# Kernel optimization log

Measured on AMD Instinct MI355X. Metric: run time of the kernel, lower is better.

Reference implementation:

```python
import jax, jax.numpy as jnp
import numpy as np

NL, D, DI, N, R, K = 4, 256, 512, 16, 16, 4  # layers, d_model, d_inner, d_state, dt_rank, conv kernel


def setup_inputs() -> dict:
    key = jax.random.key(0)
    ks = jax.random.split(key, 10)
    b, nc, nt = 8, 256, 64
    xc = jax.random.normal(ks[0], (b, nc, D), jnp.float32)
    xt = jax.random.normal(ks[1], (b, nt, D), jnp.float32)
    ln_g = jnp.ones((NL, D), jnp.float32)
    ln_b = jnp.zeros((NL, D), jnp.float32)
    W_in = jax.random.normal(ks[2], (NL, D, 2 * DI), jnp.float32) * (D ** -0.5)
    W_conv = jax.random.normal(ks[3], (NL, DI, 1, K), jnp.float32) * 0.2
    b_conv = jnp.zeros((NL, DI), jnp.float32)
    W_x = jax.random.normal(ks[4], (NL, DI, R + 2 * N), jnp.float32) * (DI ** -0.5)
    W_dt = jax.random.normal(ks[5], (NL, R, DI), jnp.float32) * (R ** -0.5)
    b_dt = jax.random.normal(ks[6], (NL, DI), jnp.float32) * 0.5 - 4.0  # softplus ~ 0.02
    A_log = jnp.broadcast_to(jnp.log(jnp.arange(1, N + 1, dtype=jnp.float32)), (NL, DI, N)).copy()
    Dp = jnp.ones((NL, DI), jnp.float32)
    W_out = jax.random.normal(ks[7], (NL, DI, D), jnp.float32) * (DI ** -0.5)
    return dict(xc=xc, xt=xt, ln_g=ln_g, ln_b=ln_b, W_in=W_in, W_conv=W_conv, b_conv=b_conv,
                W_x=W_x, W_dt=W_dt, b_dt=b_dt, A_log=A_log, Dp=Dp, W_out=W_out)


def _mamba_layer(x, g, beta, Wi, Wc, bc, Wx, Wdt, bdt, Alog, Dvec, Wo):
    # x: [B, L, D]; pre-LN residual Mamba-1 block
    mu = jnp.mean(x, axis=-1, keepdims=True)
    var = jnp.var(x, axis=-1, keepdims=True)
    h = (x - mu) * jax.lax.rsqrt(var + 1e-5) * g + beta
    xz = h @ Wi                              # [B, L, 2*DI]
    xp, z = xz[..., :DI], xz[..., DI:]
    # causal depthwise conv1d
    xcv = jax.lax.conv_general_dilated(xp.transpose(0, 2, 1), Wc, (1,), [(K - 1, 0)],
                                       feature_group_count=DI,
                                       dimension_numbers=('NCH', 'OIH', 'NCH'))
    xcv = jax.nn.silu(xcv.transpose(0, 2, 1) + bc)  # [B, L, DI]
    dbl = xcv @ Wx                           # [B, L, R+2N]
    dt = jax.nn.softplus(dbl[..., :R] @ Wdt + bdt)   # [B, L, DI]
    Bm = dbl[..., R:R + N]                   # [B, L, N]
    Cm = dbl[..., R + N:]                    # [B, L, N]
    A = -jnp.exp(Alog)                       # [DI, N]

    def step(hst, inp):
        x_t, dt_t, b_t, c_t = inp            # [B,DI],[B,DI],[B,N],[B,N]
        dA = jnp.exp(dt_t[:, :, None] * A)   # [B, DI, N]
        hst = dA * hst + (dt_t * x_t)[:, :, None] * b_t[:, None, :]
        return hst, jnp.einsum('bdn,bn->bd', hst, c_t)

    h0 = jnp.zeros((x.shape[0], DI, N), x.dtype)
    _, ys = jax.lax.scan(step, h0, (xcv.transpose(1, 0, 2), dt.transpose(1, 0, 2),
                                    Bm.transpose(1, 0, 2), Cm.transpose(1, 0, 2)))
    y = ys.transpose(1, 0, 2) + xcv * Dvec
    y = y * jax.nn.silu(z)
    return x + y @ Wo


def reference(xc, xt, ln_g, ln_b, W_in, W_conv, b_conv, W_x, W_dt, b_dt, A_log, Dp, W_out):
    b, nc, d = xc.shape
    nt = xt.shape[1]
    # replicate context per target token: [b*nt, nc+1, d]
    xr = jnp.broadcast_to(xc[:, None], (b, nt, nc, d)).reshape(b * nt, nc, d)
    x = jnp.concatenate([xr, xt.reshape(b * nt, 1, d)], axis=1)
    for i in range(NL):
        x = _mamba_layer(x, ln_g[i], ln_b[i], W_in[i], W_conv[i], b_conv[i],
                         W_x[i], W_dt[i], b_dt[i], A_log[i], Dp[i], W_out[i])
    return x[:, -1, :].reshape(b, nt, d)
```

## Files before the change

### kernel.cpp

```cpp
#include <hip/hip_runtime.h>
#include <hip/hip_bf16.h>

#define D_     256
#define TWO_DI 1024
#define DI_    512
#define NSTATE 16
#define RR     16
#define NDBL   48
#define BSEQ   8
#define NC     256
#define NCHUNK 16
#define CLEN   16
#define CTX    2048
#define TGT    512

typedef __attribute__((ext_vector_type(8))) short short8v;
typedef __attribute__((ext_vector_type(8))) unsigned short ushort8v;
typedef __attribute__((ext_vector_type(4))) float floatx4;

__device__ __forceinline__ float siluf(float x) { return x / (1.f + __expf(-x)); }
__device__ __forceinline__ float softplusf(float x) {
  return fmaxf(x, 0.f) + log1pf(__expf(-fabsf(x)));
}
__device__ __forceinline__ unsigned short f2bf(float x) {
  unsigned u = __float_as_uint(x);
  u += 0x7fffu + ((u >> 16) & 1u);
  return (unsigned short)(u >> 16);
}
__device__ __forceinline__ float bf2f(unsigned short b) {
  return __uint_as_float((unsigned)b << 16);
}

__global__ __launch_bounds__(256) void prep_all(
    const float* __restrict__ W_in, const float* __restrict__ W_o,
    const float* __restrict__ W_x, const float* __restrict__ Alog,
    const float* __restrict__ W_dt,
    unsigned short* __restrict__ Wint, unsigned short* __restrict__ Wot,
    unsigned short* __restrict__ Wxt, float* __restrict__ Aneg,
    float* __restrict__ WdtT)
{
  __shared__ float tile[32][33];
  int b = blockIdx.x;
  const float* src; unsigned short* dst; int R, C, cx, ry;
  if (b < 1024) {
    int z = b >> 8, t = b & 255; cx = t & 31; ry = t >> 5; R = 256; C = 1024;
    src = W_in + (size_t)z * R * C; dst = Wint + (size_t)z * R * C;
  } else if (b < 1536) {
    int bb = b - 1024; int z = bb >> 7, t = bb & 127; cx = t & 7; ry = t >> 3; R = 512; C = 256;
    src = W_o + (size_t)z * R * C; dst = Wot + (size_t)z * R * C;
  } else if (b < 1664) {
    int bb = b - 1536; int z = bb >> 5, t = bb & 31; cx = t & 1; ry = t >> 1; R = 512; C = 48;
    src = W_x + (size_t)z * R * C; dst = Wxt + (size_t)z * R * C;
  } else if (b < 1792) {
    int i = (b - 1664) * 256 + threadIdx.x;
    if (i < 4 * DI_ * NSTATE) Aneg[i] = -__expf(Alog[i]);
    return;
  } else {
    int i = (b - 1792) * 256 + threadIdx.x;
    int z = i >> 13, rem = i & 8191, c = rem >> 4, r = rem & 15;
    WdtT[i] = W_dt[(size_t)z * RR * DI_ + r * DI_ + c];
    return;
  }
  int c0 = cx * 32, r0 = ry * 32;
  int tx = threadIdx.x & 31, ty = threadIdx.x >> 5;
#pragma unroll
  for (int i = 0; i < 4; ++i) {
    int r = r0 + ty + i * 8;
    tile[ty + i * 8][tx] = (r < R && c0 + tx < C) ? src[(size_t)r * C + c0 + tx] : 0.f;
  }
  __syncthreads();
#pragma unroll
  for (int i = 0; i < 4; ++i) {
    int c = c0 + ty + i * 8;
    if (c < C && r0 + tx < R)
      dst[(size_t)c * R + r0 + tx] = f2bf(tile[tx][ty + i * 8]);
  }
}

__device__ __forceinline__ void ln_body(int bx, const float* __restrict__ x,
    const float* __restrict__ g, const float* __restrict__ be,
    unsigned short* __restrict__ out, int rows)
{
  int wid = threadIdx.x >> 6, lane = threadIdx.x & 63;
  int row = bx * 4 + wid;
  if (row >= rows) return;
  const float4 v = *reinterpret_cast<const float4*>(&x[(size_t)row * D_ + lane * 4]);
  float s  = v.x + v.y + v.z + v.w;
  float sq = v.x * v.x + v.y * v.y + v.z * v.z + v.w * v.w;
#pragma unroll
  for (int off = 32; off; off >>= 1) {
    s  += __shfl_xor(s, off);
    sq += __shfl_xor(sq, off);
  }
  float mu   = s * (1.f / D_);
  float var  = sq * (1.f / D_) - mu * mu;
  float rstd = rsqrtf(var + 1e-5f);
  const float4 gv = *reinterpret_cast<const float4*>(&g[lane * 4]);
  const float4 bv = *reinterpret_cast<const float4*>(&be[lane * 4]);
  ushort4 o;
  o.x = f2bf((v.x - mu) * rstd * gv.x + bv.x);
  o.y = f2bf((v.y - mu) * rstd * gv.y + bv.y);
  o.z = f2bf((v.z - mu) * rstd * gv.z + bv.z);
  o.w = f2bf((v.w - mu) * rstd * gv.w + bv.w);
  *reinterpret_cast<ushort4*>(&out[(size_t)row * D_ + lane * 4]) = o;
}

__global__ __launch_bounds__(256) void ln_kern(const float* __restrict__ x,
    const float* __restrict__ g, const float* __restrict__ be,
    unsigned short* __restrict__ out, int rows)
{
  ln_body(blockIdx.x, x, g, be, out, rows);
}

__global__ __launch_bounds__(256) void fused_ln(
    const float* __restrict__ xA, const float* __restrict__ gA,
    const float* __restrict__ bA, unsigned short* __restrict__ oA,
    const float* __restrict__ xB, const float* __restrict__ gB,
    const float* __restrict__ bB, unsigned short* __restrict__ oB)
{
  if (blockIdx.x < CTX / 4) ln_body(blockIdx.x, xA, gA, bA, oA, CTX);
  else                      ln_body(blockIdx.x - CTX / 4, xB, gB, bB, oB, TGT);
}

template<int EPI>
__device__ __forceinline__ void gemm_body(
    unsigned short (*As)[72], unsigned short (*Bs)[72], int bx, int by,
    const unsigned short* __restrict__ A, const unsigned short* __restrict__ Bt,
    const float* __restrict__ resid, float* __restrict__ C, int M, int N, int K,
    const float* __restrict__ cconv, const float* __restrict__ Wc4,
    unsigned short* __restrict__ xcv_bf, float* __restrict__ zbuf)
{
  int tid = threadIdx.x;
  int n0 = bx * 64, m0 = by * 64;
  int w = tid >> 6, lane = tid & 63;
  int lr = lane & 15, kq = lane >> 4;
  int wr = w >> 1, wc = w & 1;
  int srow = tid >> 2, schunk = (tid & 3) * 16;
  const unsigned short* Ap = &A[(size_t)(m0 + srow) * K + schunk];
  const unsigned short* Bp = &Bt[(size_t)(n0 + srow) * K + schunk];
  ushort8v a0 = *reinterpret_cast<const ushort8v*>(Ap);
  ushort8v a1 = *reinterpret_cast<const ushort8v*>(Ap + 8);
  ushort8v b0 = *reinterpret_cast<const ushort8v*>(Bp);
  ushort8v b1 = *reinterpret_cast<const ushort8v*>(Bp + 8);
  floatx4 acc[2][2] = {};
  for (int k0 = 0; k0 < K; k0 += 64) {
    __syncthreads();
    *reinterpret_cast<ushort8v*>(&As[srow][schunk])     = a0;
    *reinterpret_cast<ushort8v*>(&As[srow][schunk + 8]) = a1;
    *reinterpret_cast<ushort8v*>(&Bs[srow][schunk])     = b0;
    *reinterpret_cast<ushort8v*>(&Bs[srow][schunk + 8]) = b1;
    __syncthreads();
    if (k0 + 64 < K) {
      a0 = *reinterpret_cast<const ushort8v*>(Ap + k0 + 64);
      a1 = *reinterpret_cast<const ushort8v*>(Ap + k0 + 72);
      b0 = *reinterpret_cast<const ushort8v*>(Bp + k0 + 64);
      b1 = *reinterpret_cast<const ushort8v*>(Bp + k0 + 72);
    }
#pragma unroll
    for (int ks = 0; ks < 2; ++ks) {
      short8v af[2], bf2v[2];
#pragma unroll
      for (int f = 0; f < 2; ++f)
        af[f] = *reinterpret_cast<const short8v*>(&As[wr * 32 + f * 16 + lr][ks * 32 + kq * 8]);
#pragma unroll
      for (int g2 = 0; g2 < 2; ++g2)
        bf2v[g2] = *reinterpret_cast<const short8v*>(&Bs[wc * 32 + g2 * 16 + lr][ks * 32 + kq * 8]);
#pragma unroll
      for (int f = 0; f < 2; ++f)
#pragma unroll
        for (int g2 = 0; g2 < 2; ++g2)
          acc[f][g2] = __builtin_amdgcn_mfma_f32_16x16x32_bf16(af[f], bf2v[g2], acc[f][g2], 0, 0, 0);
    }
  }
#pragma unroll
  for (int f = 0; f < 2; ++f)
#pragma unroll
    for (int g2 = 0; g2 < 2; ++g2) {
      int col = n0 + wc * 32 + g2 * 16 + lr;
#pragma unroll
      for (int r = 0; r < 4; ++r) {
        int row = m0 + wr * 32 + f * 16 + kq * 4 + r;
        float v = acc[f][g2][r];
        if (EPI == 0) {
          if (resid) v += resid[(size_t)row * N + col];
          C[(size_t)row * N + col] = v;
        } else {
          int b = row >> 6;
          if (col < DI_) {
            float sv = siluf(cconv[b * DI_ + col] + v * Wc4[col * 4 + 3]);
            xcv_bf[(size_t)row * DI_ + col] = f2bf(sv);
          } else {
            zbuf[(size_t)row * DI_ + (col - DI_)] = v;
          }
        }
      }
    }
}

template<int EPI>
__global__ __launch_bounds__(256) void gemm_bf16(
    const unsigned short* __restrict__ A, const unsigned short* __restrict__ Bt,
    const float* __restrict__ resid, float* __restrict__ C, int M, int N, int K,
    const float* __restrict__ cconv, const float* __restrict__ Wc4,
    unsigned short* __restrict__ xcv_bf, float* __restrict__ zbuf)
{
  __shared__ unsigned short As[64][72];
  __shared__ unsigned short Bs[64][72];
  gemm_body<EPI>(As, Bs, blockIdx.x, blockIdx.y, A, Bt, resid, C, M, N, K,
                 cconv, Wc4, xcv_bf, zbuf);
}

__global__ __launch_bounds__(256) void fused_gemm_in(
    const unsigned short* __restrict__ Aa, const unsigned short* __restrict__ Bta,
    float* __restrict__ Ca,
    const unsigned short* __restrict__ Ab, const unsigned short* __restrict__ Btb,
    const float* __restrict__ cconv, const float* __restrict__ Wc4,
    unsigned short* __restrict__ xcv_bf, float* __restrict__ zbuf)
{
  __shared__ unsigned short As[64][72];
  __shared__ unsigned short Bs[64][72];
  int f = blockIdx.x;
  if (f < 512)
    gemm_body<0>(As, Bs, f & 15, f >> 4, Aa, Bta, nullptr, Ca, CTX, TWO_DI, D_,
                 nullptr, nullptr, nullptr, nullptr);
  else {
    f -= 512;
    gemm_body<1>(As, Bs, f & 15, f >> 4, Ab, Btb, nullptr, nullptr, TGT, TWO_DI, D_,
                 cconv, Wc4, xcv_bf, zbuf);
  }
}

__device__ __forceinline__ void gemm_s_body(int bx, int by,
    const unsigned short* __restrict__ A, const unsigned short* __restrict__ Bt,
    const float* __restrict__ resid, float* __restrict__ C, int M, int N, int K)
{
  __shared__ unsigned short As[32][72];
  __shared__ unsigned short Bs[32][72];
  int tid = threadIdx.x;
  int n0 = bx * 32, m0 = by * 32;
  int w = tid >> 6, lane = tid & 63;
  int lr = lane & 15, kq = lane >> 4;
  int wr = w >> 1, wc = w & 1;
  int srow = tid >> 3, schunk = (tid & 7) * 8;
  const unsigned short* Ap = &A[(size_t)(m0 + srow) * K + schunk];
  const unsigned short* Bp = &Bt[(size_t)(n0 + srow) * K + schunk];
  ushort8v a0 = *reinterpret_cast<const ushort8v*>(Ap);
  ushort8v b0 = *reinterpret_cast<const ushort8v*>(Bp);
  floatx4 acc = {};
  for (int k0 = 0; k0 < K; k0 += 64) {
    __syncthreads();
    *reinterpret_cast<ushort8v*>(&As[srow][schunk]) = a0;
    *reinterpret_cast<ushort8v*>(&Bs[srow][schunk]) = b0;
    __syncthreads();
    if (k0 + 64 < K) {
      a0 = *reinterpret_cast<const ushort8v*>(Ap + k0 + 64);
      b0 = *reinterpret_cast<const ushort8v*>(Bp + k0 + 64);
    }
#pragma unroll
    for (int ks = 0; ks < 2; ++ks) {
      short8v af = *reinterpret_cast<const short8v*>(&As[wr * 16 + lr][ks * 32 + kq * 8]);
      short8v bf = *reinterpret_cast<const short8v*>(&Bs[wc * 16 + lr][ks * 32 + kq * 8]);
      acc = __builtin_amdgcn_mfma_f32_16x16x32_bf16(af, bf, acc, 0, 0, 0);
    }
  }
  int col = n0 + wc * 16 + lr;
#pragma unroll
  for (int r = 0; r < 4; ++r) {
    int row = m0 + wr * 16 + kq * 4 + r;
    float v = acc[r];
    if (resid) v += resid[(size_t)row * N + col];
    C[(size_t)row * N + col] = v;
  }
}

__global__ __launch_bounds__(256) void gemm_s(
    const unsigned short* __restrict__ A, const unsigned short* __restrict__ Bt,
    const float* __restrict__ resid, float* __restrict__ C, int M, int N, int K)
{
  gemm_s_body(blockIdx.x, blockIdx.y, A, Bt, resid, C, M, N, K);
}

__device__ __forceinline__ void conv_body_lean(int blk,
    const float* __restrict__ xz, const float* __restrict__ Wc,
    const float* __restrict__ bc, const unsigned short* __restrict__ Wxt,
    const float* __restrict__ WdtT, const float* __restrict__ bdt,
    unsigned short* __restrict__ xcvb, float* __restrict__ dtb,
    float* __restrict__ dblg, float* __restrict__ cconv)
{
  __shared__ unsigned short xcs[16][528];
  __shared__ float dbl_s[16][48];
  int seq = blk >> 4, ch = blk & 15;
  int tok0 = blk * 16;
  int tid = threadIdx.x;
  int base = ch * 16;
#pragma unroll
  for (int hh = 0; hh < 2; ++hh) {
    int c = tid + hh * 256;
    const float4 wv = *reinterpret_cast<const float4*>(&Wc[c * 4]);
    float bcv = bc[c];
    const float* xzs = &xz[(size_t)(seq * NC) * TWO_DI + c];
    float r[19];
#pragma unroll
    for (int i = 0; i < 19; ++i) {
      int tl = base - 3 + i;
      r[i] = (tl >= 0) ? xzs[(size_t)tl * TWO_DI] : 0.f;
    }
#pragma unroll
    for (int t = 0; t < 16; ++t) {
      float acc = bcv + r[t] * wv.x + r[t + 1] * wv.y + r[t + 2] * wv.z + r[t + 3] * wv.w;
      unsigned short sv = f2bf(siluf(acc));
      xcs[t][c] = sv;
      xcvb[(size_t)(tok0 + t) * DI_ + c] = sv;
    }
    if (ch == 15)
      cconv[seq * DI_ + c] = bcv + r[16] * wv.x + r[17] * wv.y + r[18] * wv.z;
  }
  __syncthreads();
  int w = tid >> 6, lane = tid & 63, lr = lane & 15, kq = lane >> 4;
  if (w < 3) {
    floatx4 acc = {};
#pragma unroll
    for (int kc = 0; kc < 16; ++kc) {
      short8v bb = *reinterpret_cast<const short8v*>(&Wxt[(size_t)(w * 16 + lr) * DI_ + kc * 32 + kq * 8]);
      short8v aa = *reinterpret_cast<const short8v*>(&xcs[lr][kc * 32 + kq * 8]);
      acc = __builtin_amdgcn_mfma_f32_16x16x32_bf16(aa, bb, acc, 0, 0, 0);
    }
#pragma unroll
    for (int r2 = 0; r2 < 4; ++r2) {
      int t = kq * 4 + r2, col = w * 16 + lr;
      dbl_s[t][col] = acc[r2];
      dblg[(size_t)(tok0 + t) * NDBL + col] = acc[r2];
    }
  }
  __syncthreads();
#pragma unroll
  for (int hh = 0; hh < 2; ++hh) {
    int c = tid + hh * 256;
    float wr_[16];
    const float4* wt4 = reinterpret_cast<const float4*>(&WdtT[c * 16]);
#pragma unroll
    for (int q = 0; q < 4; ++q) {
      float4 v4 = wt4[q];
      wr_[q * 4] = v4.x; wr_[q * 4 + 1] = v4.y; wr_[q * 4 + 2] = v4.z; wr_[q * 4 + 3] = v4.w;
    }
    float bv = bdt[c];
#pragma unroll
    for (int t = 0; t < 16; ++t) {
      float accd = bv;
#pragma unroll
      for (int r2 = 0; r2 < 16; ++r2) accd += dbl_s[t][r2] * wr_[r2];
      dtb[(size_t)(tok0 + t) * DI_ + c] = softplusf(accd);
    }
  }
}

__global__ __launch_bounds__(256) void conv_lean_kern(
    const float* __restrict__ xz, const float* __restrict__ Wc,
    const float* __restrict__ bc, const unsigned short* __restrict__ Wxt,
    const float* __restrict__ WdtT, const float* __restrict__ bdt,
    unsigned short* __restrict__ xcvb, float* __restrict__ dtb,
    float* __restrict__ dblg, float* __restrict__ cconv)
{
  conv_body_lean(blockIdx.x, xz, Wc, bc, Wxt, WdtT, bdt, xcvb, dtb, dblg, cconv);
}

__device__ __forceinline__ void sp_body(int b,
    const float* __restrict__ dblg, const unsigned short* __restrict__ xcvb,
    const float* __restrict__ dtb, const float* __restrict__ Aneg,
    float* __restrict__ Sb, float* __restrict__ Pb)
{
  int dg = b & 31, sc = b >> 5;
  int tid = threadIdx.x;
  int tt = tid >> 4, cc = tid & 15;
  int tok0 = sc * CLEN;
  __shared__ float dts[16][17], xs[16][17], Bs[16][17];
  dts[tt][cc] = dtb[(size_t)(tok0 + tt) * DI_ + dg * 16 + cc];
  xs[tt][cc]  = bf2f(xcvb[(size_t)(tok0 + tt) * DI_ + dg * 16 + cc]);
  Bs[tt][cc]  = dblg[(size_t)(tok0 + tt) * NDBL + RR + cc];
  __syncthreads();
  int dl = tt, n = cc;
  int d = dg * 16 + dl;
  float A = Aneg[d * NSTATE + n];
  float Bn[16];
#pragma unroll
  for (int t = 0; t < CLEN; ++t) Bn[t] = Bs[t][n];
  float h = 0.f, p = 1.f;
#pragma unroll
  for (int t = 0; t < CLEN; ++t) {
    float dtv = dts[t][dl];
    float dA  = __expf(dtv * A);
    h = fmaf(dA, h, dtv * xs[t][dl] * Bn[t]);
    p *= dA;
  }
  size_t o = ((size_t)sc * DI_ + d) * NSTATE + n;
  Sb[o] = h; Pb[o] = p;
}

__global__ __launch_bounds__(256) void sp_kern(
    const float* __restrict__ dblg, const unsigned short* __restrict__ xcvb,
    const float* __restrict__ dtb, const float* __restrict__ Aneg,
    float* __restrict__ Sb, float* __restrict__ Pb)
{
  sp_body(blockIdx.x, dblg, xcvb, dtb, Aneg, Sb, Pb);
}

__global__ __launch_bounds__(256) void fused_sp_gout(
    const unsigned short* __restrict__ Ag, const unsigned short* __restrict__ Btg,
    const float* __restrict__ residg, float* __restrict__ Cg,
    const float* __restrict__ dblg, const unsigned short* __restrict__ xcvb,
    const float* __restrict__ dtb, const float* __restrict__ Aneg,
    float* __restrict__ Sb, float* __restrict__ Pb)
{
  if (blockIdx.x < 128) {
    int f = blockIdx.x;
    gemm_s_body(f & 7, f >> 3, Ag, Btg, residg, Cg, TGT, D_, DI_);
  } else {
    sp_body(blockIdx.x - 128, dblg, xcvb, dtb, Aneg, Sb, Pb);
  }
}

__global__ __launch_bounds__(256) void scan_fin(
    const float* __restrict__ dblg, const unsigned short* __restrict__ xcvb,
    const float* __restrict__ xz, const float* __restrict__ dtb,
    const float* __restrict__ Sb, const float* __restrict__ Pb,
    const float* __restrict__ Aneg, const float* __restrict__ Dp,
    unsigned short* __restrict__ yb, float* __restrict__ hstate)
{
  int b = blockIdx.x;
  int dg = b & 31, sc = b >> 5;
  int seq = sc >> 4, chunk = sc & 15;
  int tid = threadIdx.x;
  int tt = tid >> 4, cc = tid & 15;
  int tok0 = sc * CLEN;
  __shared__ float dts[16][17], xs[16][17], zs[16][17], Bs[16][17], Cs[16][17], ys[16][17];
  dts[tt][cc] = dtb[(size_t)(tok0 + tt) * DI_ + dg * 16 + cc];
  xs[tt][cc]  = bf2f(xcvb[(size_t)(tok0 + tt) * DI_ + dg * 16 + cc]);
  zs[tt][cc]  = xz[(size_t)(tok0 + tt) * TWO_DI + DI_ + dg * 16 + cc];
  Bs[tt][cc]  = dblg[(size_t)(tok0 + tt) * NDBL + RR + cc];
  Cs[tt][cc]  = dblg[(size_t)(tok0 + tt) * NDBL + RR + NSTATE + cc];
  __syncthreads();
  int dl = tt, n = cc;
  int d = dg * 16 + dl;
  float A  = Aneg[d * NSTATE + n];
  float Dv = Dp[d];
  float Bn[16], Cn[16];
#pragma unroll
  for (int t = 0; t < CLEN; ++t) { Bn[t] = Bs[t][n]; Cn[t] = Cs[t][n]; }
  float h = 0.f;
  for (int c2 = 0; c2 < chunk; ++c2) {
    size_t o = ((size_t)(seq * NCHUNK + c2) * DI_ + d) * NSTATE + n;
    h = fmaf(Pb[o], h, Sb[o]);
  }
#pragma unroll
  for (int t = 0; t < CLEN; ++t) {
    float dtv = dts[t][dl];
    float xv  = xs[t][dl];
    float dA  = __expf(dtv * A);
    h = fmaf(dA, h, dtv * xv * Bn[t]);
    float p = h * Cn[t];
    p += __shfl_xor(p, 1); p += __shfl_xor(p, 2);
    p += __shfl_xor(p, 4); p += __shfl_xor(p, 8);
    if (n == 0) ys[t][dl] = (p + xv * Dv) * siluf(zs[t][dl]);
  }
  __syncthreads();
  yb[(size_t)(tok0 + tt) * DI_ + dg * 16 + cc] = f2bf(ys[tt][cc]);
  if (chunk == NCHUNK - 1)
    hstate[(size_t)seq * DI_ * NSTATE + d * NSTATE + n] = h;
}

__device__ __forceinline__ void ssm_body(int blk,
    const unsigned short* __restrict__ xcv_bf, const float* __restrict__ zbuf,
    const unsigned short* __restrict__ Wx, const float* __restrict__ WdtT_l,
    const float* __restrict__ bdt_l, const float* __restrict__ An_l,
    const float* __restrict__ Dp_l, const float* __restrict__ hs,
    unsigned short* __restrict__ ybf)
{
  __shared__ float dbl_s[16][48];
  int tg = blk >> 3, cg = blk & 7;
  int tok0 = tg * 16;
  int b = tg >> 2;
  int tid = threadIdx.x;
  int w = tid >> 6, lane = tid & 63, lr = lane & 15, kq = lane >> 4;
  if (w < 3) {
    floatx4 acc = {};
#pragma unroll
    for (int kc = 0; kc < 16; ++kc) {
      short8v bb = *reinterpret_cast<const short8v*>(&Wx[(size_t)(w * 16 + lr) * DI_ + kc * 32 + kq * 8]);
      short8v aa = *reinterpret_cast<const short8v*>(&xcv_bf[(size_t)(tok0 + lr) * DI_ + kc * 32 + kq * 8]);
      acc = __builtin_amdgcn_mfma_f32_16x16x32_bf16(aa, bb, acc, 0, 0, 0);
    }
#pragma unroll
    for (int r = 0; r < 4; ++r)
      dbl_s[kq * 4 + r][w * 16 + lr] = acc[r];
  }
  __syncthreads();
  int c = cg * 64 + (tid & 63);
  int t0 = (tid >> 6) * 4;
  float wdt_r[16], An[16], hr[16];
  const float4* wt4 = reinterpret_cast<const float4*>(&WdtT_l[c * 16]);
  const float4* An4 = reinterpret_cast<const float4*>(&An_l[c * NSTATE]);
  const float4* hr4 = reinterpret_cast<const float4*>(&hs[(size_t)b * DI_ * NSTATE + c * NSTATE]);
#pragma unroll
  for (int q = 0; q < 4; ++q) {
    float4 wv = wt4[q]; wdt_r[q*4]=wv.x; wdt_r[q*4+1]=wv.y; wdt_r[q*4+2]=wv.z; wdt_r[q*4+3]=wv.w;
    float4 a = An4[q]; An[q*4]=a.x; An[q*4+1]=a.y; An[q*4+2]=a.z; An[q*4+3]=a.w;
    float4 hv = hr4[q]; hr[q*4]=hv.x; hr[q*4+1]=hv.y; hr[q*4+2]=hv.z; hr[q*4+3]=hv.w;
  }
  float Dv = Dp_l[c], bv = bdt_l[c];
#pragma unroll
  for (int tt = 0; tt < 4; ++tt) {
    int t = t0 + tt;
    float accd = bv;
#pragma unroll
    for (int r = 0; r < 16; ++r) accd += dbl_s[t][r] * wdt_r[r];
    float dtv = softplusf(accd);
    float xv = bf2f(xcv_bf[(size_t)(tok0 + t) * DI_ + c]);
    float coef = dtv * xv;
    float y = 0.f;
#pragma unroll
    for (int n = 0; n < 16; ++n) {
      float hn = fmaf(__expf(dtv * An[n]), hr[n], coef * dbl_s[t][RR + n]);
      y = fmaf(hn, dbl_s[t][RR + NSTATE + n], y);
    }
    float yv = (y + xv * Dv) * siluf(zbuf[(size_t)(tok0 + t) * DI_ + c]);
    ybf[(size_t)(tok0 + t) * DI_ + c] = f2bf(yv);
  }
}

__global__ __launch_bounds__(256) void tgt_ssm2(
    const unsigned short* __restrict__ xcv_bf, const float* __restrict__ zbuf,
    const unsigned short* __restrict__ Wx, const float* __restrict__ WdtT_l,
    const float* __restrict__ bdt_l, const float* __restrict__ An_l,
    const float* __restrict__ Dp_l, const float* __restrict__ hs,
    unsigned short* __restrict__ ybf)
{
  ssm_body(blockIdx.x, xcv_bf, zbuf, Wx, WdtT_l, bdt_l, An_l, Dp_l, hs, ybf);
}

__global__ __launch_bounds__(256) void fused_conv_ssm(
    const float* __restrict__ xz, const float* __restrict__ Wc,
    const float* __restrict__ bc, const unsigned short* __restrict__ WxtA,
    const float* __restrict__ WdtTA, const float* __restrict__ bdtA,
    unsigned short* __restrict__ xcvb, float* __restrict__ dtb,
    float* __restrict__ dblg, float* __restrict__ cconv,
    const unsigned short* __restrict__ xcv_bfB, const float* __restrict__ zbufB,
    const unsigned short* __restrict__ WxB, const float* __restrict__ WdtTB,
    const float* __restrict__ bdtB, const float* __restrict__ AnB,
    const float* __restrict__ DpB, const float* __restrict__ hsB,
    unsigned short* __restrict__ ybfB)
{
  if (blockIdx.x < BSEQ * NCHUNK)
    conv_body_lean(blockIdx.x, xz, Wc, bc, WxtA, WdtTA, bdtA,
                   xcvb, dtb, dblg, cconv);
  else
    ssm_body(blockIdx.x - BSEQ * NCHUNK, xcv_bfB, zbufB, WxB, WdtTB, bdtB,
             AnB, DpB, hsB, ybfB);
}

extern "C" void kernel_launch(void* const* d_in, const int* in_sizes, int n_in,
                              void* d_out, int out_size, void* d_ws, size_t ws_size,
                              hipStream_t stream)
{
  const float* xc   = (const float*)d_in[0];
  const float* xt   = (const float*)d_in[1];
  const float* ln_g = (const float*)d_in[2];
  const float* ln_b = (const float*)d_in[3];
  const float* W_in = (const float*)d_in[4];
  const float* W_cv = (const float*)d_in[5];
  const float* b_cv = (const float*)d_in[6];
  const float* W_x  = (const float*)d_in[7];
  const float* W_dt = (const float*)d_in[8];
  const float* b_dt = (const float*)d_in[9];
  const float* Alog = (const float*)d_in[10];
  const float* Dp   = (const float*)d_in[11];
  const float* W_o  = (const float*)d_in[12];
  float* out = (float*)d_out;

  float* ws = (float*)d_ws;
  size_t off = 0;
  auto alloc = [&](size_t n) { float* p = ws + off; off += n; return p; };
  float* xz     = alloc((size_t)CTX * TWO_DI);
  float* dtb    = alloc((size_t)CTX * DI_);
  float* dblg   = alloc((size_t)CTX * NDBL);
  float* xcur   = alloc((size_t)CTX * D_);
  float* Sb     = alloc((size_t)BSEQ * NCHUNK * DI_ * NSTATE);
  float* Pb     = alloc((size_t)BSEQ * NCHUNK * DI_ * NSTATE);
  float* cconvT = alloc((size_t)4 * BSEQ * DI_);
  float* hst    = alloc((size_t)4 * BSEQ * DI_ * NSTATE);
  float* Aneg   = alloc((size_t)4 * DI_ * NSTATE);
  float* WdtT   = alloc((size_t)4 * DI_ * RR);
  float* zbufB  = alloc((size_t)TGT * DI_);
  float* xtb    = alloc((size_t)TGT * D_);
  unsigned short* hbuf_bf = (unsigned short*)alloc((size_t)CTX * D_ / 2);
  unsigned short* hbufB   = (unsigned short*)alloc((size_t)TGT * D_ / 2);
  unsigned short* xcvb    = (unsigned short*)alloc((size_t)CTX * DI_ / 2);
  unsigned short* yb_bf   = (unsigned short*)alloc((size_t)CTX * DI_ / 2);
  unsigned short* xcv_bfB = (unsigned short*)alloc((size_t)TGT * DI_ / 2);
  unsigned short* y_bfB   = (unsigned short*)alloc((size_t)TGT * DI_ / 2);
  unsigned short* Wint    = (unsigned short*)alloc((size_t)4 * TWO_DI * D_ / 2);
  unsigned short* Wot     = (unsigned short*)alloc((size_t)4 * D_ * DI_ / 2);
  unsigned short* Wxt     = (unsigned short*)alloc((size_t)4 * NDBL * DI_ / 2);
  if (off * sizeof(float) > ws_size) return;

  prep_all<<<1920, 256, 0, stream>>>(W_in, W_o, W_x, Alog, W_dt,
                                     Wint, Wot, Wxt, Aneg, WdtT);

  ln_kern<<<CTX / 4, 256, 0, stream>>>(xc, ln_g, ln_b, hbuf_bf, CTX);
  gemm_bf16<0><<<dim3(TWO_DI / 64, CTX / 64), 256, 0, stream>>>(
      hbuf_bf, Wint, nullptr, xz, CTX, TWO_DI, D_, nullptr, nullptr, nullptr, nullptr);
  conv_lean_kern<<<BSEQ * NCHUNK, 256, 0, stream>>>(
      xz, W_cv, b_cv, Wxt, WdtT, b_dt, xcvb, dtb, dblg, cconvT);
  sp_kern<<<BSEQ * NCHUNK * 32, 256, 0, stream>>>(dblg, xcvb, dtb, Aneg, Sb, Pb);
  scan_fin<<<BSEQ * NCHUNK * 32, 256, 0, stream>>>(
      dblg, xcvb, xz, dtb, Sb, Pb, Aneg, Dp, yb_bf, hst);
  gemm_bf16<0><<<dim3(D_ / 64, CTX / 64), 256, 0, stream>>>(
      yb_bf, Wot, xc, xcur, CTX, D_, DI_, nullptr, nullptr, nullptr, nullptr);

  for (int l = 0; l < 3; ++l) {
    int la = l + 1;
    const float* xinB = (l == 0) ? xt : xtb;
    fused_ln<<<CTX / 4 + TGT / 4, 256, 0, stream>>>(
        xcur, ln_g + la * D_, ln_b + la * D_, hbuf_bf,
        xinB, ln_g + l * D_,  ln_b + l * D_,  hbufB);
    fused_gemm_in<<<512 + 128, 256, 0, stream>>>(
        hbuf_bf, Wint + (size_t)la * TWO_DI * D_, xz,
        hbufB,   Wint + (size_t)l * TWO_DI * D_,
        cconvT + (size_t)l * BSEQ * DI_, W_cv + l * DI_ * 4, xcv_bfB, zbufB);
    fused_conv_ssm<<<BSEQ * NCHUNK + 256, 256, 0, stream>>>(
        xz, W_cv + la * DI_ * 4, b_cv + la * DI_, Wxt + (size_t)la * NDBL * DI_,
        WdtT + (size_t)la * DI_ * RR, b_dt + la * DI_,
        xcvb, dtb, dblg, cconvT + (size_t)la * BSEQ * DI_,
        xcv_bfB, zbufB, Wxt + (size_t)l * NDBL * DI_, WdtT + (size_t)l * DI_ * RR,
        b_dt + l * DI_, Aneg + l * DI_ * NSTATE, Dp + l * DI_,
        hst + (size_t)l * BSEQ * DI_ * NSTATE, y_bfB);
    fused_sp_gout<<<128 + BSEQ * NCHUNK * 32, 256, 0, stream>>>(
        y_bfB, Wot + (size_t)l * D_ * DI_, xinB, xtb,
        dblg, xcvb, dtb, Aneg + la * DI_ * NSTATE, Sb, Pb);
    scan_fin<<<BSEQ * NCHUNK * 32, 256, 0, stream>>>(
        dblg, xcvb, xz, dtb, Sb, Pb, Aneg + la * DI_ * NSTATE, Dp + la * DI_,
        yb_bf, hst + (size_t)la * BSEQ * DI_ * NSTATE);
    if (la < 3)
      gemm_bf16<0><<<dim3(D_ / 64, CTX / 64), 256, 0, stream>>>(
          yb_bf, Wot + (size_t)la * D_ * DI_, xcur, xcur, CTX, D_, DI_,
          nullptr, nullptr, nullptr, nullptr);
  }

  ln_kern<<<TGT / 4, 256, 0, stream>>>(xtb, ln_g + 3 * D_, ln_b + 3 * D_, hbufB, TGT);
  gemm_bf16<1><<<dim3(TWO_DI / 64, TGT / 64), 256, 0, stream>>>(
      hbufB, Wint + (size_t)3 * TWO_DI * D_, nullptr, nullptr, TGT, TWO_DI, D_,
      cconvT + (size_t)3 * BSEQ * DI_, W_cv + 3 * DI_ * 4, xcv_bfB, zbufB);
  tgt_ssm2<<<256, 256, 0, stream>>>(xcv_bfB, zbufB,
      Wxt + (size_t)3 * NDBL * DI_, WdtT + (size_t)3 * DI_ * RR, b_dt + 3 * DI_,
      Aneg + 3 * DI_ * NSTATE, Dp + 3 * DI_,
      hst + (size_t)3 * BSEQ * DI_ * NSTATE, y_bfB);
  gemm_s<<<dim3(D_ / 32, TGT / 32), 256, 0, stream>>>(
      y_bfB, Wot + (size_t)3 * D_ * DI_, xtb, out, TGT, D_, DI_);
}
```

Before: 306.3 us.

## Fuse layernorm into input GEMM and replace chunked scan with sequential full scan

LayerNorm is folded into the input-projection GEMM: each block recomputes row mean and variance from fp32 activations and normalizes on the fly while staging A tiles, which removes the separate LN launches and the bf16 hidden buffers. The two-pass chunked scan (per-chunk partial states, then a prefix combine) is replaced by one kernel per sequence and channel group that walks all 16 chunks in order, prefetching the next chunk's inputs into registers. This removes a kernel launch and the Sb/Pb state traffic per layer. In exchange it cuts scan parallelism from 4096 to 256 blocks and makes every N-tile block of the GEMM recompute the LN statistics.

```diff
diff --git a/kernel.cpp b/kernel.cpp
--- a/kernel.cpp
+++ b/kernel.cpp
@@ -77,61 +77,161 @@
   }
 }
 
-__device__ __forceinline__ void ln_body(int bx, const float* __restrict__ x,
-    const float* __restrict__ g, const float* __restrict__ be,
-    unsigned short* __restrict__ out, int rows)
-{
-  int wid = threadIdx.x >> 6, lane = threadIdx.x & 63;
-  int row = bx * 4 + wid;
-  if (row >= rows) return;
-  const float4 v = *reinterpret_cast<const float4*>(&x[(size_t)row * D_ + lane * 4]);
-  float s  = v.x + v.y + v.z + v.w;
-  float sq = v.x * v.x + v.y * v.y + v.z * v.z + v.w * v.w;
-#pragma unroll
-  for (int off = 32; off; off >>= 1) {
-    s  += __shfl_xor(s, off);
-    sq += __shfl_xor(sq, off);
-  }
-  float mu   = s * (1.f / D_);
-  float var  = sq * (1.f / D_) - mu * mu;
-  float rstd = rsqrtf(var + 1e-5f);
-  const float4 gv = *reinterpret_cast<const float4*>(&g[lane * 4]);
-  const float4 bv = *reinterpret_cast<const float4*>(&be[lane * 4]);
-  ushort4 o;
-  o.x = f2bf((v.x - mu) * rstd * gv.x + bv.x);
-  o.y = f2bf((v.y - mu) * rstd * gv.y + bv.y);
-  o.z = f2bf((v.z - mu) * rstd * gv.z + bv.z);
-  o.w = f2bf((v.w - mu) * rstd * gv.w + bv.w);
-  *reinterpret_cast<ushort4*>(&out[(size_t)row * D_ + lane * 4]) = o;
-}
-
-__global__ __launch_bounds__(256) void ln_kern(const float* __restrict__ x,
-    const float* __restrict__ g, const float* __restrict__ be,
-    unsigned short* __restrict__ out, int rows)
-{
-  ln_body(blockIdx.x, x, g, be, out, rows);
-}
-
-__global__ __launch_bounds__(256) void fused_ln(
-    const float* __restrict__ xA, const float* __restrict__ gA,
-    const float* __restrict__ bA, unsigned short* __restrict__ oA,
-    const float* __restrict__ xB, const float* __restrict__ gB,
-    const float* __restrict__ bB, unsigned short* __restrict__ oB)
-{
-  if (blockIdx.x < CTX / 4) ln_body(blockIdx.x, xA, gA, bA, oA, CTX);
-  else                      ln_body(blockIdx.x - CTX / 4, xB, gB, bB, oB, TGT);
-}
-
 template<int EPI>
-__device__ __forceinline__ void gemm_body(
-    unsigned short (*As)[72], unsigned short (*Bs)[72], int bx, int by,
-    const unsigned short* __restrict__ A, const unsigned short* __restrict__ Bt,
-    const float* __restrict__ resid, float* __restrict__ C, int M, int N, int K,
+__device__ __forceinline__ void gemm_in_ln_body(
+    unsigned short (*As)[72], unsigned short (*Bs)[72],
+    float* gs, float* bs, int bx, int by,
+    const float* __restrict__ X, const float* __restrict__ g,
+    const float* __restrict__ be, const unsigned short* __restrict__ Bt,
+    float* __restrict__ C, int N,
     const float* __restrict__ cconv, const float* __restrict__ Wc4,
     unsigned short* __restrict__ xcv_bf, float* __restrict__ zbuf)
 {
+  const int K = D_;
   int tid = threadIdx.x;
   int n0 = bx * 64, m0 = by * 64;
+  int w = tid >> 6, lane = tid & 63;
+  int lr = lane & 15, kq = lane >> 4;
+  int wr = w >> 1, wc = w & 1;
+  int srow = tid >> 2, schunk = (tid & 3) * 16;
+  const float* Apf = &X[(size_t)(m0 + srow) * K];
+  {
+    const float4* xr = reinterpret_cast<const float4*>(&Apf[(tid & 3) * 64]);
+    float s = 0.f, sq = 0.f;
+#pragma unroll
+    for (int i = 0; i < 16; ++i) {
+      float4 v = xr[i];
+      s += v.x + v.y + v.z + v.w;
+      sq += v.x * v.x + v.y * v.y + v.z * v.z + v.w * v.w;
+    }
+    s += __shfl_xor(s, 1);  s += __shfl_xor(s, 2);
+    sq += __shfl_xor(sq, 1); sq += __shfl_xor(sq, 2);
+    float mu = s * (1.f / K);
+    float rstd = rsqrtf(sq * (1.f / K) - mu * mu + 1e-5f);
+    gs[tid] = g[tid]; bs[tid] = be[tid];
+    const unsigned short* Bp = &Bt[(size_t)(n0 + srow) * K + schunk];
+    float4 af[4];
+#pragma unroll
+    for (int i = 0; i < 4; ++i)
+      af[i] = *reinterpret_cast<const float4*>(&Apf[schunk + i * 4]);
+    ushort8v b0 = *reinterpret_cast<const ushort8v*>(Bp);
+    ushort8v b1 = *reinterpret_cast<const ushort8v*>(Bp + 8);
+    floatx4 acc[2][2] = {};
+    for (int k0 = 0; k0 < K; k0 += 64) {
+      __syncthreads();
+      {
+        int cb = k0 + schunk;
+        ushort8v o0, o1;
+#pragma unroll
+        for (int i = 0; i < 4; ++i) {
+          float4 v = af[i];
+          unsigned short e0 = f2bf((v.x - mu) * rstd * gs[cb + i * 4 + 0] + bs[cb + i * 4 + 0]);
+          unsigned short e1 = f2bf((v.y - mu) * rstd * gs[cb + i * 4 + 1] + bs[cb + i * 4 + 1]);
+          unsigned short e2 = f2bf((v.z - mu) * rstd * gs[cb + i * 4 + 2] + bs[cb + i * 4 + 2]);
+          unsigned short e3 = f2bf((v.w - mu) * rstd * gs[cb + i * 4 + 3] + bs[cb + i * 4 + 3]);
+          if (i < 2) { o0[i*4] = (short)e0; o0[i*4+1] = (short)e1; o0[i*4+2] = (short)e2; o0[i*4+3] = (short)e3; }
+          else { int j = (i-2)*4; o1[j] = (short)e0; o1[j+1] = (short)e1; o1[j+2] = (short)e2; o1[j+3] = (short)e3; }
+        }
+        *reinterpret_cast<ushort8v*>(&As[srow][schunk])     = o0;
+        *reinterpret_cast<ushort8v*>(&As[srow][schunk + 8]) = o1;
+      }
+      *reinterpret_cast<ushort8v*>(&Bs[srow][schunk])     = b0;
+      *reinterpret_cast<ushort8v*>(&Bs[srow][schunk + 8]) = b1;
+      __syncthreads();
+      if (k0 + 64 < K) {
+#pragma unroll
+        for (int i = 0; i < 4; ++i)
+          af[i] = *reinterpret_cast<const float4*>(&Apf[k0 + 64 + schunk + i * 4]);
+        b0 = *reinterpret_cast<const ushort8v*>(Bp + k0 + 64);
+        b1 = *reinterpret_cast<const ushort8v*>(Bp + k0 + 72);
+      }
+#pragma unroll
+      for (int ks = 0; ks < 2; ++ks) {
+        short8v af2[2], bf2v[2];
+#pragma unroll
+        for (int f = 0; f < 2; ++f)
+          af2[f] = *reinterpret_cast<const short8v*>(&As[wr * 32 + f * 16 + lr][ks * 32 + kq * 8]);
+#pragma unroll
+        for (int g2 = 0; g2 < 2; ++g2)
+          bf2v[g2] = *reinterpret_cast<const short8v*>(&Bs[wc * 32 + g2 * 16 + lr][ks * 32 + kq * 8]);
+#pragma unroll
+        for (int f = 0; f < 2; ++f)
+#pragma unroll
+          for (int g2 = 0; g2 < 2; ++g2)
+            acc[f][g2] = __builtin_amdgcn_mfma_f32_16x16x32_bf16(af2[f], bf2v[g2], acc[f][g2], 0, 0, 0);
+      }
+    }
+#pragma unroll
+    for (int f = 0; f < 2; ++f)
+#pragma unroll
+      for (int g2 = 0; g2 < 2; ++g2) {
+        int col = n0 + wc * 32 + g2 * 16 + lr;
+#pragma unroll
+        for (int r = 0; r < 4; ++r) {
+          int row = m0 + wr * 32 + f * 16 + kq * 4 + r;
+          float v = acc[f][g2][r];
+          if (EPI == 0) {
+            C[(size_t)row * N + col] = v;
+          } else {
+            int bb = row >> 6;
+            if (col < DI_) {
+              float sv = siluf(cconv[bb * DI_ + col] + v * Wc4[col * 4 + 3]);
+              xcv_bf[(size_t)row * DI_ + col] = f2bf(sv);
+            } else {
+              zbuf[(size_t)row * DI_ + (col - DI_)] = v;
+            }
+          }
+        }
+      }
+  }
+}
+
+template<int EPI>
+__global__ __launch_bounds__(256) void gemm_in_ln(
+    const float* __restrict__ X, const float* __restrict__ g,
+    const float* __restrict__ be, const unsigned short* __restrict__ Bt,
+    float* __restrict__ C,
+    const float* __restrict__ cconv, const float* __restrict__ Wc4,
+    unsigned short* __restrict__ xcv_bf, float* __restrict__ zbuf)
+{
+  __shared__ unsigned short As[64][72];
+  __shared__ unsigned short Bs[64][72];
+  __shared__ float gs[256], bs[256];
+  gemm_in_ln_body<EPI>(As, Bs, gs, bs, blockIdx.x, blockIdx.y, X, g, be, Bt,
+                       C, TWO_DI, cconv, Wc4, xcv_bf, zbuf);
+}
+
+__global__ __launch_bounds__(256) void fused_gemm_in_ln(
+    const float* __restrict__ Xa, const float* __restrict__ ga,
+    const float* __restrict__ ba, float* __restrict__ Ca,
+    const unsigned short* __restrict__ Bta,
+    const float* __restrict__ Xb, const float* __restrict__ gb,
+    const float* __restrict__ bb, const unsigned short* __restrict__ Btb,
+    const float* __restrict__ cconv, const float* __restrict__ Wc4,
+    unsigned short* __restrict__ xcv_bf, float* __restrict__ zbuf)
+{
+  __shared__ unsigned short As[64][72];
+  __shared__ unsigned short Bs[64][72];
+  __shared__ float gs[256], bs[256];
+  int f = blockIdx.x;
+  if (f < 512)
+    gemm_in_ln_body<0>(As, Bs, gs, bs, f & 15, f >> 4, Xa, ga, ba, Bta,
+                       Ca, TWO_DI, nullptr, nullptr, nullptr, nullptr);
+  else {
+    f -= 512;
+    gemm_in_ln_body<1>(As, Bs, gs, bs, f & 15, f >> 4, Xb, gb, bb, Btb,
+                       nullptr, TWO_DI, cconv, Wc4, xcv_bf, zbuf);
+  }
+}
+
+__global__ __launch_bounds__(256) void gemm_out(
+    const unsigned short* __restrict__ A, const unsigned short* __restrict__ Bt,
+    const float* __restrict__ resid, float* __restrict__ C, int N, int K)
+{
+  __shared__ unsigned short As[64][72];
+  __shared__ unsigned short Bs[64][72];
+  int tid = threadIdx.x;
+  int n0 = blockIdx.x * 64, m0 = blockIdx.y * 64;
   int w = tid >> 6, lane = tid & 63;
   int lr = lane & 15, kq = lane >> 4;
   int wr = w >> 1, wc = w & 1;
@@ -180,59 +280,15 @@
 #pragma unroll
       for (int r = 0; r < 4; ++r) {
         int row = m0 + wr * 32 + f * 16 + kq * 4 + r;
-        float v = acc[f][g2][r];
-        if (EPI == 0) {
-          if (resid) v += resid[(size_t)row * N + col];
-          C[(size_t)row * N + col] = v;
-        } else {
-          int b = row >> 6;
-          if (col < DI_) {
-            float sv = siluf(cconv[b * DI_ + col] + v * Wc4[col * 4 + 3]);
-            xcv_bf[(size_t)row * DI_ + col] = f2bf(sv);
-          } else {
-            zbuf[(size_t)row * DI_ + (col - DI_)] = v;
-          }
-        }
+        float v = acc[f][g2][r] + resid[(size_t)row * N + col];
+        C[(size_t)row * N + col] = v;
       }
     }
-}
-
-template<int EPI>
-__global__ __launch_bounds__(256) void gemm_bf16(
-    const unsigned short* __restrict__ A, const unsigned short* __restrict__ Bt,
-    const float* __restrict__ resid, float* __restrict__ C, int M, int N, int K,
-    const float* __restrict__ cconv, const float* __restrict__ Wc4,
-    unsigned short* __restrict__ xcv_bf, float* __restrict__ zbuf)
-{
-  __shared__ unsigned short As[64][72];
-  __shared__ unsigned short Bs[64][72];
-  gemm_body<EPI>(As, Bs, blockIdx.x, blockIdx.y, A, Bt, resid, C, M, N, K,
-                 cconv, Wc4, xcv_bf, zbuf);
-}
-
-__global__ __launch_bounds__(256) void fused_gemm_in(
-    const unsigned short* __restrict__ Aa, const unsigned short* __restrict__ Bta,
-    float* __restrict__ Ca,
-    const unsigned short* __restrict__ Ab, const unsigned short* __restrict__ Btb,
-    const float* __restrict__ cconv, const float* __restrict__ Wc4,
-    unsigned short* __restrict__ xcv_bf, float* __restrict__ zbuf)
-{
-  __shared__ unsigned short As[64][72];
-  __shared__ unsigned short Bs[64][72];
-  int f = blockIdx.x;
-  if (f < 512)
-    gemm_body<0>(As, Bs, f & 15, f >> 4, Aa, Bta, nullptr, Ca, CTX, TWO_DI, D_,
-                 nullptr, nullptr, nullptr, nullptr);
-  else {
-    f -= 512;
-    gemm_body<1>(As, Bs, f & 15, f >> 4, Ab, Btb, nullptr, nullptr, TGT, TWO_DI, D_,
-                 cconv, Wc4, xcv_bf, zbuf);
-  }
 }
 
 __device__ __forceinline__ void gemm_s_body(int bx, int by,
     const unsigned short* __restrict__ A, const unsigned short* __restrict__ Bt,
-    const float* __restrict__ resid, float* __restrict__ C, int M, int N, int K)
+    const float* __restrict__ resid, float* __restrict__ C, int N, int K)
 {
   __shared__ unsigned short As[32][72];
   __shared__ unsigned short Bs[32][72];
@@ -267,17 +323,16 @@
 #pragma unroll
   for (int r = 0; r < 4; ++r) {
     int row = m0 + wr * 16 + kq * 4 + r;
-    float v = acc[r];
-    if (resid) v += resid[(size_t)row * N + col];
+    float v = acc[r] + resid[(size_t)row * N + col];
     C[(size_t)row * N + col] = v;
   }
 }
 
 __global__ __launch_bounds__(256) void gemm_s(
     const unsigned short* __restrict__ A, const unsigned short* __restrict__ Bt,
-    const float* __restrict__ resid, float* __restrict__ C, int M, int N, int K)
-{
-  gemm_s_body(blockIdx.x, blockIdx.y, A, Bt, resid, C, M, N, K);
+    const float* __restrict__ resid, float* __restrict__ C, int N, int K)
+{
+  gemm_s_body(blockIdx.x, blockIdx.y, A, Bt, resid, C, N, K);
 }
 
 __device__ __forceinline__ void conv_body_lean(int blk,
@@ -364,108 +419,88 @@
   conv_body_lean(blockIdx.x, xz, Wc, bc, Wxt, WdtT, bdt, xcvb, dtb, dblg, cconv);
 }
 
-__device__ __forceinline__ void sp_body(int b,
+__device__ __forceinline__ void fullscan_body(int b,
     const float* __restrict__ dblg, const unsigned short* __restrict__ xcvb,
-    const float* __restrict__ dtb, const float* __restrict__ Aneg,
-    float* __restrict__ Sb, float* __restrict__ Pb)
-{
-  int dg = b & 31, sc = b >> 5;
+    const float* __restrict__ xz, const float* __restrict__ dtb,
+    const float* __restrict__ Aneg, const float* __restrict__ Dp,
+    unsigned short* __restrict__ yb, float* __restrict__ hstate)
+{
+  __shared__ float dts[16][17], xs[16][17], zs[16][17], Bsh[16][17], Csh[16][17], ys[16][17];
+  int dg = b & 31, seq = b >> 5;
   int tid = threadIdx.x;
   int tt = tid >> 4, cc = tid & 15;
-  int tok0 = sc * CLEN;
-  __shared__ float dts[16][17], xs[16][17], Bs[16][17];
-  dts[tt][cc] = dtb[(size_t)(tok0 + tt) * DI_ + dg * 16 + cc];
-  xs[tt][cc]  = bf2f(xcvb[(size_t)(tok0 + tt) * DI_ + dg * 16 + cc]);
-  Bs[tt][cc]  = dblg[(size_t)(tok0 + tt) * NDBL + RR + cc];
-  __syncthreads();
-  int dl = tt, n = cc;
-  int d = dg * 16 + dl;
-  float A = Aneg[d * NSTATE + n];
-  float Bn[16];
-#pragma unroll
-  for (int t = 0; t < CLEN; ++t) Bn[t] = Bs[t][n];
-  float h = 0.f, p = 1.f;
-#pragma unroll
-  for (int t = 0; t < CLEN; ++t) {
-    float dtv = dts[t][dl];
-    float dA  = __expf(dtv * A);
-    h = fmaf(dA, h, dtv * xs[t][dl] * Bn[t]);
-    p *= dA;
-  }
-  size_t o = ((size_t)sc * DI_ + d) * NSTATE + n;
-  Sb[o] = h; Pb[o] = p;
-}
-
-__global__ __launch_bounds__(256) void sp_kern(
-    const float* __restrict__ dblg, const unsigned short* __restrict__ xcvb,
-    const float* __restrict__ dtb, const float* __restrict__ Aneg,
-    float* __restrict__ Sb, float* __restrict__ Pb)
-{
-  sp_body(blockIdx.x, dblg, xcvb, dtb, Aneg, Sb, Pb);
-}
-
-__global__ __launch_bounds__(256) void fused_sp_gout(
-    const unsigned short* __restrict__ Ag, const unsigned short* __restrict__ Btg,
-    const float* __restrict__ residg, float* __restrict__ Cg,
-    const float* __restrict__ dblg, const unsigned short* __restrict__ xcvb,
-    const float* __restrict__ dtb, const float* __restrict__ Aneg,
-    float* __restrict__ Sb, float* __restrict__ Pb)
-{
-  if (blockIdx.x < 128) {
-    int f = blockIdx.x;
-    gemm_s_body(f & 7, f >> 3, Ag, Btg, residg, Cg, TGT, D_, DI_);
-  } else {
-    sp_body(blockIdx.x - 128, dblg, xcvb, dtb, Aneg, Sb, Pb);
-  }
-}
-
-__global__ __launch_bounds__(256) void scan_fin(
-    const float* __restrict__ dblg, const unsigned short* __restrict__ xcvb,
-    const float* __restrict__ xz, const float* __restrict__ dtb,
-    const float* __restrict__ Sb, const float* __restrict__ Pb,
-    const float* __restrict__ Aneg, const float* __restrict__ Dp,
-    unsigned short* __restrict__ yb, float* __restrict__ hstate)
-{
-  int b = blockIdx.x;
-  int dg = b & 31, sc = b >> 5;
-  int seq = sc >> 4, chunk = sc & 15;
-  int tid = threadIdx.x;
-  int tt = tid >> 4, cc = tid & 15;
-  int tok0 = sc * CLEN;
-  __shared__ float dts[16][17], xs[16][17], zs[16][17], Bs[16][17], Cs[16][17], ys[16][17];
-  dts[tt][cc] = dtb[(size_t)(tok0 + tt) * DI_ + dg * 16 + cc];
-  xs[tt][cc]  = bf2f(xcvb[(size_t)(tok0 + tt) * DI_ + dg * 16 + cc]);
-  zs[tt][cc]  = xz[(size_t)(tok0 + tt) * TWO_DI + DI_ + dg * 16 + cc];
-  Bs[tt][cc]  = dblg[(size_t)(tok0 + tt) * NDBL + RR + cc];
-  Cs[tt][cc]  = dblg[(size_t)(tok0 + tt) * NDBL + RR + NSTATE + cc];
-  __syncthreads();
   int dl = tt, n = cc;
   int d = dg * 16 + dl;
   float A  = Aneg[d * NSTATE + n];
   float Dv = Dp[d];
-  float Bn[16], Cn[16];
-#pragma unroll
-  for (int t = 0; t < CLEN; ++t) { Bn[t] = Bs[t][n]; Cn[t] = Cs[t][n]; }
   float h = 0.f;
-  for (int c2 = 0; c2 < chunk; ++c2) {
-    size_t o = ((size_t)(seq * NCHUNK + c2) * DI_ + d) * NSTATE + n;
-    h = fmaf(Pb[o], h, Sb[o]);
-  }
-#pragma unroll
-  for (int t = 0; t < CLEN; ++t) {
-    float dtv = dts[t][dl];
-    float xv  = xs[t][dl];
-    float dA  = __expf(dtv * A);
-    h = fmaf(dA, h, dtv * xv * Bn[t]);
-    float p = h * Cn[t];
-    p += __shfl_xor(p, 1); p += __shfl_xor(p, 2);
-    p += __shfl_xor(p, 4); p += __shfl_xor(p, 8);
-    if (n == 0) ys[t][dl] = (p + xv * Dv) * siluf(zs[t][dl]);
-  }
-  __syncthreads();
-  yb[(size_t)(tok0 + tt) * DI_ + dg * 16 + cc] = f2bf(ys[tt][cc]);
-  if (chunk == NCHUNK - 1)
-    hstate[(size_t)seq * DI_ * NSTATE + d * NSTATE + n] = h;
+  float r_dt, r_x, r_z, r_B, r_C;
+  {
+    int tok = seq * NC + tt;
+    size_t rowD = (size_t)tok * DI_ + dg * 16 + cc;
+    r_dt = dtb[rowD];
+    r_x  = bf2f(xcvb[rowD]);
+    r_z  = xz[(size_t)tok * TWO_DI + DI_ + dg * 16 + cc];
+    r_B  = dblg[(size_t)tok * NDBL + RR + cc];
+    r_C  = dblg[(size_t)tok * NDBL + RR + NSTATE + cc];
+  }
+  for (int ch = 0; ch < 16; ++ch) {
+    dts[tt][cc] = r_dt; xs[tt][cc] = r_x; zs[tt][cc] = r_z;
+    Bsh[tt][cc] = r_B; Csh[tt][cc] = r_C;
+    __syncthreads();
+    if (ch < 15) {
+      int tok = seq * NC + (ch + 1) * 16 + tt;
+      size_t rowD = (size_t)tok * DI_ + dg * 16 + cc;
+      r_dt = dtb[rowD];
+      r_x  = bf2f(xcvb[rowD]);
+      r_z  = xz[(size_t)tok * TWO_DI + DI_ + dg * 16 + cc];
+      r_B  = dblg[(size_t)tok * NDBL + RR + cc];
+      r_C  = dblg[(size_t)tok * NDBL + RR + NSTATE + cc];
+    }
+    float Bn[16], Cn[16];
+#pragma unroll
+    for (int t = 0; t < CLEN; ++t) { Bn[t] = Bsh[t][n]; Cn[t] = Csh[t][n]; }
+#pragma unroll
+    for (int t = 0; t < CLEN; ++t) {
+      float dtv = dts[t][dl];
+      float xv  = xs[t][dl];
+      float dA  = __expf(dtv * A);
+      h = fmaf(dA, h, dtv * xv * Bn[t]);
+      float p = h * Cn[t];
+      p += __shfl_xor(p, 1); p += __shfl_xor(p, 2);
+      p += __shfl_xor(p, 4); p += __shfl_xor(p, 8);
+      if (n == 0) ys[t][dl] = (p + xv * Dv) * siluf(zs[t][dl]);
+    }
+    __syncthreads();
+    int tok0 = seq * NC + ch * 16;
+    yb[(size_t)(tok0 + tt) * DI_ + dg * 16 + cc] = f2bf(ys[tt][cc]);
+  }
+  hstate[(size_t)seq * DI_ * NSTATE + d * NSTATE + n] = h;
+}
+
+__global__ __launch_bounds__(256) void fullscan_kern(
+    const float* __restrict__ dblg, const unsigned short* __restrict__ xcvb,
+    const float* __restrict__ xz, const float* __restrict__ dtb,
+    const float* __restrict__ Aneg, const float* __restrict__ Dp,
+    unsigned short* __restrict__ yb, float* __restrict__ hstate)
+{
+  fullscan_body(blockIdx.x, dblg, xcvb, xz, dtb, Aneg, Dp, yb, hstate);
+}
+
+__global__ __launch_bounds__(256) void fused_scan_gout(
+    const unsigned short* __restrict__ Ag, const unsigned short* __restrict__ Btg,
+    const float* __restrict__ residg, float* __restrict__ Cg,
+    const float* __restrict__ dblg, const unsigned short* __restrict__ xcvb,
+    const float* __restrict__ xz, const float* __restrict__ dtb,
+    const float* __restrict__ Aneg, const float* __restrict__ Dp,
+    unsigned short* __restrict__ yb, float* __restrict__ hstate)
+{
+  if (blockIdx.x < 128) {
+    int f = blockIdx.x;
+    gemm_s_body(f & 7, f >> 3, Ag, Btg, residg, Cg, D_, DI_);
+  } else {
+    fullscan_body(blockIdx.x - 128, dblg, xcvb, xz, dtb, Aneg, Dp, yb, hstate);
+  }
 }
 
 __device__ __forceinline__ void ssm_body(int blk,
@@ -583,16 +618,12 @@
   float* dtb    = alloc((size_t)CTX * DI_);
   float* dblg   = alloc((size_t)CTX * NDBL);
   float* xcur   = alloc((size_t)CTX * D_);
-  float* Sb     = alloc((size_t)BSEQ * NCHUNK * DI_ * NSTATE);
-  float* Pb     = alloc((size_t)BSEQ * NCHUNK * DI_ * NSTATE);
   float* cconvT = alloc((size_t)4 * BSEQ * DI_);
   float* hst    = alloc((size_t)4 * BSEQ * DI_ * NSTATE);
   float* Aneg   = alloc((size_t)4 * DI_ * NSTATE);
   float* WdtT   = alloc((size_t)4 * DI_ * RR);
   float* zbufB  = alloc((size_t)TGT * DI_);
   float* xtb    = alloc((size_t)TGT * D_);
-  unsigned short* hbuf_bf = (unsigned short*)alloc((size_t)CTX * D_ / 2);
-  unsigned short* hbufB   = (unsigned short*)alloc((size_t)TGT * D_ / 2);
   unsigned short* xcvb    = (unsigned short*)alloc((size_t)CTX * DI_ / 2);
   unsigned short* yb_bf   = (unsigned short*)alloc((size_t)CTX * DI_ / 2);
   unsigned short* xcv_bfB = (unsigned short*)alloc((size_t)TGT * DI_ / 2);
@@ -605,26 +636,20 @@
   prep_all<<<1920, 256, 0, stream>>>(W_in, W_o, W_x, Alog, W_dt,
                                      Wint, Wot, Wxt, Aneg, WdtT);
 
-  ln_kern<<<CTX / 4, 256, 0, stream>>>(xc, ln_g, ln_b, hbuf_bf, CTX);
-  gemm_bf16<0><<<dim3(TWO_DI / 64, CTX / 64), 256, 0, stream>>>(
-      hbuf_bf, Wint, nullptr, xz, CTX, TWO_DI, D_, nullptr, nullptr, nullptr, nullptr);
+  gemm_in_ln<0><<<dim3(16, CTX / 64), 256, 0, stream>>>(
+      xc, ln_g, ln_b, Wint, xz, nullptr, nullptr, nullptr, nullptr);
   conv_lean_kern<<<BSEQ * NCHUNK, 256, 0, stream>>>(
       xz, W_cv, b_cv, Wxt, WdtT, b_dt, xcvb, dtb, dblg, cconvT);
-  sp_kern<<<BSEQ * NCHUNK * 32, 256, 0, stream>>>(dblg, xcvb, dtb, Aneg, Sb, Pb);
-  scan_fin<<<BSEQ * NCHUNK * 32, 256, 0, stream>>>(
-      dblg, xcvb, xz, dtb, Sb, Pb, Aneg, Dp, yb_bf, hst);
-  gemm_bf16<0><<<dim3(D_ / 64, CTX / 64), 256, 0, stream>>>(
-      yb_bf, Wot, xc, xcur, CTX, D_, DI_, nullptr, nullptr, nullptr, nullptr);
+  fullscan_kern<<<256, 256, 0, stream>>>(dblg, xcvb, xz, dtb, Aneg, Dp, yb_bf, hst);
+  gemm_out<<<dim3(D_ / 64, CTX / 64), 256, 0, stream>>>(
+      yb_bf, Wot, xc, xcur, D_, DI_);
 
   for (int l = 0; l < 3; ++l) {
     int la = l + 1;
     const float* xinB = (l == 0) ? xt : xtb;
-    fused_ln<<<CTX / 4 + TGT / 4, 256, 0, stream>>>(
-        xcur, ln_g + la * D_, ln_b + la * D_, hbuf_bf,
-        xinB, ln_g + l * D_,  ln_b + l * D_,  hbufB);
-    fused_gemm_in<<<512 + 128, 256, 0, stream>>>(
-        hbuf_bf, Wint + (size_t)la * TWO_DI * D_, xz,
-        hbufB,   Wint + (size_t)l * TWO_DI * D_,
+    fused_gemm_in_ln<<<512 + 128, 256, 0, stream>>>(
+        xcur, ln_g + la * D_, ln_b + la * D_, xz, Wint + (size_t)la * TWO_DI * D_,
+        xinB, ln_g + l * D_, ln_b + l * D_, Wint + (size_t)l * TWO_DI * D_,
         cconvT + (size_t)l * BSEQ * DI_, W_cv + l * DI_ * 4, xcv_bfB, zbufB);
     fused_conv_ssm<<<BSEQ * NCHUNK + 256, 256, 0, stream>>>(
         xz, W_cv + la * DI_ * 4, b_cv + la * DI_, Wxt + (size_t)la * NDBL * DI_,
@@ -633,26 +658,22 @@
         xcv_bfB, zbufB, Wxt + (size_t)l * NDBL * DI_, WdtT + (size_t)l * DI_ * RR,
         b_dt + l * DI_, Aneg + l * DI_ * NSTATE, Dp + l * DI_,
         hst + (size_t)l * BSEQ * DI_ * NSTATE, y_bfB);
-    fused_sp_gout<<<128 + BSEQ * NCHUNK * 32, 256, 0, stream>>>(
+    fused_scan_gout<<<128 + 256, 256, 0, stream>>>(
         y_bfB, Wot + (size_t)l * D_ * DI_, xinB, xtb,
-        dblg, xcvb, dtb, Aneg + la * DI_ * NSTATE, Sb, Pb);
-    scan_fin<<<BSEQ * NCHUNK * 32, 256, 0, stream>>>(
-        dblg, xcvb, xz, dtb, Sb, Pb, Aneg + la * DI_ * NSTATE, Dp + la * DI_,
+        dblg, xcvb, xz, dtb, Aneg + la * DI_ * NSTATE, Dp + la * DI_,
         yb_bf, hst + (size_t)la * BSEQ * DI_ * NSTATE);
     if (la < 3)
-      gemm_bf16<0><<<dim3(D_ / 64, CTX / 64), 256, 0, stream>>>(
-          yb_bf, Wot + (size_t)la * D_ * DI_, xcur, xcur, CTX, D_, DI_,
-          nullptr, nullptr, nullptr, nullptr);
-  }
-
-  ln_kern<<<TGT / 4, 256, 0, stream>>>(xtb, ln_g + 3 * D_, ln_b + 3 * D_, hbufB, TGT);
-  gemm_bf16<1><<<dim3(TWO_DI / 64, TGT / 64), 256, 0, stream>>>(
-      hbufB, Wint + (size_t)3 * TWO_DI * D_, nullptr, nullptr, TGT, TWO_DI, D_,
+      gemm_out<<<dim3(D_ / 64, CTX / 64), 256, 0, stream>>>(
+          yb_bf, Wot + (size_t)la * D_ * DI_, xcur, xcur, D_, DI_);
+  }
+
+  gemm_in_ln<1><<<dim3(16, TGT / 64), 256, 0, stream>>>(
+      xtb, ln_g + 3 * D_, ln_b + 3 * D_, Wint + (size_t)3 * TWO_DI * D_, nullptr,
       cconvT + (size_t)3 * BSEQ * DI_, W_cv + 3 * DI_ * 4, xcv_bfB, zbufB);
   tgt_ssm2<<<256, 256, 0, stream>>>(xcv_bfB, zbufB,
       Wxt + (size_t)3 * NDBL * DI_, WdtT + (size_t)3 * DI_ * RR, b_dt + 3 * DI_,
       Aneg + 3 * DI_ * NSTATE, Dp + 3 * DI_,
       hst + (size_t)3 * BSEQ * DI_ * NSTATE, y_bfB);
   gemm_s<<<dim3(D_ / 32, TGT / 32), 256, 0, stream>>>(
-      y_bfB, Wot + (size_t)3 * D_ * DI_, xtb, out, TGT, D_, DI_);
-}
+      y_bfB, Wot + (size_t)3 * D_ * DI_, xtb, out, D_, DI_);
+}
```

Result: slower. 475.1 us (+55.1%).
